# Optimization experiments

Measured on AMD Instinct MI355X. Metric: run time of the kernel, lower is better.

The kernel has to match this reference:

```python
import jax, jax.numpy as jnp
import numpy as np

B, T, E = 128, 8, 52
S, R, L = 2048, 512, 4
VOCAB = 512


def setup_inputs() -> dict:
    key = jax.random.key(0)
    ks = jax.random.split(key, 16)
    enc_len = jax.random.randint(ks[5], (B,), 0, S, dtype=jnp.int32)
    enc_len = jnp.maximum(enc_len, 1)  # ragged lengths >= 1
    return {
        "featEmbed": jax.random.normal(ks[0], (B, T, E), jnp.float32),
        "labelsEmbed": jax.random.normal(ks[1], (B, T, E), jnp.float32),
        "encoder_outputs": jax.random.normal(ks[2], (B, S, R), jnp.float32),
        "h_n": jax.random.normal(ks[3], (B, R), jnp.float32),
        "mask": jax.random.randint(ks[4], (B, T), 0, 2, dtype=jnp.int32),
        "enc_len": enc_len,
        "emb_feat_table": jax.random.normal(ks[6], (VOCAB, E), jnp.float32) * 0.1,
        "W_fc_pool": jax.random.normal(ks[7], (L, R), jnp.float32) * (1.0 / np.sqrt(R)),
        "W_reg": jax.random.normal(ks[8], (L, R), jnp.float32) * (1.0 / np.sqrt(R)),
        "b_reg": jax.random.normal(ks[9], (L,), jnp.float32) * 0.01,
        "W_ih": jax.random.normal(ks[10], (3 * R, 2 * E), jnp.float32) * (1.0 / np.sqrt(2 * E)),
        "W_hh": jax.random.normal(ks[11], (3 * R, R), jnp.float32) * (1.0 / np.sqrt(R)),
        "b_ih": jax.random.normal(ks[12], (3 * R,), jnp.float32) * 0.01,
        "b_hh": jax.random.normal(ks[13], (3 * R,), jnp.float32) * 0.01,
    }


# label -> feature-vocab remap (dict d in original forward)
REMAP = jnp.array([175, 176, 44, 173], dtype=jnp.int32)


def _gru_cell(x, h, W_ih, W_hh, b_ih, b_hh):
    # PyTorch nn.GRUCell semantics
    gi = x @ W_ih.T + b_ih  # [B, 3R]
    gh = h @ W_hh.T + b_hh
    i_r, i_z, i_n = jnp.split(gi, 3, axis=1)
    h_r, h_z, h_nn = jnp.split(gh, 3, axis=1)
    r = jax.nn.sigmoid(i_r + h_r)
    z = jax.nn.sigmoid(i_z + h_z)
    n = jnp.tanh(i_n + r * h_nn)
    return (1.0 - z) * n + z * h


def reference(featEmbed, labelsEmbed, encoder_outputs, h_n, mask, enc_len,
              emb_feat_table, W_fc_pool, W_reg, b_reg, W_ih, W_hh, b_ih, b_hh):
    S_ = encoder_outputs.shape[1]
    # Ragged max-pool over valid encoder positions (replaces per-sample AdaptiveMaxPool1d loop)
    valid = jnp.arange(S_)[None, :] < enc_len[:, None]          # [B, S]
    neg = jnp.finfo(encoder_outputs.dtype).min
    code_pool = jnp.max(jnp.where(valid[:, :, None], encoder_outputs, neg), axis=1)  # [B, R]
    a = code_pool @ W_fc_pool.T                                  # [B, L]; constant over t

    def step(h, inp):
        x, bmi_t, m = inp                                        # [B,E], [B,E], [B]
        bmi_h = h @ W_reg.T + b_reg + a                          # [B, L]
        bmi_prob = jax.nn.sigmoid(bmi_h)
        bmi_label = jnp.argmax(bmi_prob, axis=1)                 # [B]
        label_dict = REMAP[bmi_label]                            # host-dict remap, vectorized
        bmi_label_enc = emb_feat_table[label_dict]               # [B, E]
        mf = m.astype(x.dtype)[:, None]
        bmi = bmi_t * mf + (1.0 - mf) * bmi_label_enc
        h_new = _gru_cell(jnp.concatenate([x, bmi], axis=1), h, W_ih, W_hh, b_ih, b_hh)
        return h_new, (bmi_label, bmi_prob, bmi_h, label_dict)

    xs = (jnp.swapaxes(featEmbed, 0, 1),    # [T,B,E]
          jnp.swapaxes(labelsEmbed, 0, 1),  # [T,B,E]
          mask.T)                            # [T,B]
    _, (dec_output, dec_prob, disc_input, kl_input) = jax.lax.scan(step, h_n, xs)
    L_ = dec_prob.shape[-1]
    # dec_output: [T,B] labels; dec_prob: [T,B,L]; disc_input: [T*B,L]; kl_input: [T*B]
    return dec_output, dec_prob, disc_input.reshape(-1, L_), kl_input.reshape(-1)
```

## Files before the change

kernel.cpp:

```cpp
#include <hip/hip_runtime.h>
#include <float.h>
#include <math.h>


#define B_ 128
#define T_ 8
#define E_ 52
#define S_ 2048
#define R_ 512
#define L_ 4
#define GR_ 1536
#define KX_ 104
#define NCHUNK 16
#define SCHUNK (S_ / NCHUNK)
#define NQ_ 154
#define XQ_ 26

__device__ __constant__ int c_remap[4] = {175, 176, 44, 173};

__device__ __forceinline__ float sigmoidf(float x) { return 1.0f / (1.0f + expf(-x)); }
__device__ __forceinline__ float dot4(float4 w, float4 x, float a) {
    a = fmaf(w.x, x.x, a);
    a = fmaf(w.y, x.y, a);
    a = fmaf(w.z, x.z, a);
    a = fmaf(w.w, x.w, a);
    return a;
}

__global__ void k_maxpool(const float* __restrict__ enc, const int* __restrict__ enc_len,
                          float4* __restrict__ partial) {
    int c = blockIdx.x;
    int b = blockIdx.y;
    int t = threadIdx.x;
    int len = enc_len[b];
    int s0 = c * SCHUNK;
    int s1 = min(s0 + SCHUNK, len);
    float4 m = make_float4(-FLT_MAX, -FLT_MAX, -FLT_MAX, -FLT_MAX);
    const float4* base = (const float4*)(enc + (size_t)b * S_ * R_);
    for (int s = s0; s < s1; ++s) {
        float4 v = base[(size_t)s * (R_ / 4) + t];
        m.x = fmaxf(m.x, v.x);
        m.y = fmaxf(m.y, v.y);
        m.z = fmaxf(m.z, v.z);
        m.w = fmaxf(m.w, v.w);
    }
    partial[((size_t)b * NCHUNK + c) * (R_ / 4) + t] = m;
}

__global__ void k_pool_a(const float* __restrict__ partial, const float* __restrict__ W_fc,
                         float* __restrict__ a_out) {
    int b = blockIdx.x;
    int tid = threadIdx.x;
    __shared__ float cp[R_];
    for (int r = tid; r < R_; r += 256) {
        float m = -FLT_MAX;
        const float* p = partial + (size_t)b * NCHUNK * R_ + r;
        #pragma unroll
        for (int c = 0; c < NCHUNK; ++c) m = fmaxf(m, p[c * R_]);
        cp[r] = m;
    }
    __syncthreads();
    float p0 = 0.f, p1 = 0.f, p2 = 0.f, p3 = 0.f;
    for (int r = tid; r < R_; r += 256) {
        float v = cp[r];
        p0 = fmaf(v, W_fc[0 * R_ + r], p0);
        p1 = fmaf(v, W_fc[1 * R_ + r], p1);
        p2 = fmaf(v, W_fc[2 * R_ + r], p2);
        p3 = fmaf(v, W_fc[3 * R_ + r], p3);
    }
    #pragma unroll
    for (int off = 32; off > 0; off >>= 1) {
        p0 += __shfl_down(p0, off);
        p1 += __shfl_down(p1, off);
        p2 += __shfl_down(p2, off);
        p3 += __shfl_down(p3, off);
    }
    __shared__ float red[4][4];
    int wv = tid >> 6, lane = tid & 63;
    if (lane == 0) { red[wv][0] = p0; red[wv][1] = p1; red[wv][2] = p2; red[wv][3] = p3; }
    __syncthreads();
    if (tid < 4) {
        a_out[b * L_ + tid] = red[0][tid] + red[1][tid] + red[2][tid] + red[3][tid];
    }
}

__global__ void k_pack(const float* __restrict__ Wih, const float* __restrict__ Whh,
                       float4* __restrict__ Wp) {
    int qd = blockIdx.x;
    int rr = threadIdx.x;
    #pragma unroll
    for (int g = 0; g < 3; ++g) {
        int row = g * 512 + rr;
        float4 v;
        if (qd < XQ_) v = *(const float4*)(Wih + (size_t)row * KX_ + 4 * qd);
        else          v = *(const float4*)(Whh + (size_t)row * R_  + 4 * (qd - XQ_));
        Wp[((size_t)qd * 3 + g) * 512 + rr] = v;
    }
}

__global__ void __launch_bounds__(1024, 1) k_step(
        const float* __restrict__ h, const float* __restrict__ W_reg,
        const float* __restrict__ b_reg, const float* __restrict__ a_vec,
        const float* __restrict__ featEmbed, const float* __restrict__ labelsEmbed,
        const int* __restrict__ mask, const float* __restrict__ emb_table,
        const float4* __restrict__ Wp, const float* __restrict__ b_ih,
        const float* __restrict__ b_hh,
        int t, float* __restrict__ h_out, float* __restrict__ out) {
    int tid = threadIdx.x;
    int lane = tid & 63;
    int w = tid >> 6;
    int b0 = blockIdx.y * 4;
    int rr = blockIdx.x * 64 + lane;

    __shared__ __align__(16) float xs[4][KX_];
    __shared__ __align__(16) float hs[4][R_];
    __shared__ float red[8][64][17];

    if (w >= 4 && w < 8) {
        int bi = w - 4;
        const float4* src = (const float4*)(h + (size_t)(b0 + bi) * R_);
        float4* dst = (float4*)hs[bi];
        dst[lane] = src[lane];
        dst[lane + 64] = src[lane + 64];
    }

    if (w < 4) {
        int bp = b0 + w;
        const float* hb = h + (size_t)bp * R_;
        float p0 = 0.f, p1 = 0.f, p2 = 0.f, p3 = 0.f;
        #pragma unroll
        for (int r = lane; r < R_; r += 64) {
            float v = hb[r];
            p0 = fmaf(v, W_reg[r], p0);
            p1 = fmaf(v, W_reg[512 + r], p1);
            p2 = fmaf(v, W_reg[1024 + r], p2);
            p3 = fmaf(v, W_reg[1536 + r], p3);
        }
        #pragma unroll
        for (int off = 32; off > 0; off >>= 1) {
            p0 += __shfl_down(p0, off);
            p1 += __shfl_down(p1, off);
            p2 += __shfl_down(p2, off);
            p3 += __shfl_down(p3, off);
        }
        p0 = __shfl(p0, 0); p1 = __shfl(p1, 0); p2 = __shfl(p2, 0); p3 = __shfl(p3, 0);
        float bh[4];
        bh[0] = p0 + b_reg[0] + a_vec[bp * 4 + 0];
        bh[1] = p1 + b_reg[1] + a_vec[bp * 4 + 1];
        bh[2] = p2 + b_reg[2] + a_vec[bp * 4 + 2];
        bh[3] = p3 + b_reg[3] + a_vec[bp * 4 + 3];
        float pr[4];
        #pragma unroll
        for (int l = 0; l < 4; ++l) pr[l] = sigmoidf(bh[l]);
        int best = 0;
        float bv = pr[0];
        #pragma unroll
        for (int l = 1; l < 4; ++l) {
            if (pr[l] > bv) { bv = pr[l]; best = l; }
        }
        int ld = c_remap[best];
        if (blockIdx.x == 0 && lane == 0) {
            out[t * B_ + bp] = (float)best;
            #pragma unroll
            for (int l = 0; l < 4; ++l) {
                out[1024 + (t * B_ + bp) * 4 + l] = pr[l];
                out[5120 + (t * B_ + bp) * 4 + l] = bh[l];
            }
            out[9216 + t * B_ + bp] = (float)ld;
        }
        if (lane < E_) {
            xs[w][lane] = featEmbed[bp * (T_ * E_) + t * E_ + lane];
            int m = mask[bp * T_ + t];
            xs[w][E_ + lane] = m ? labelsEmbed[bp * (T_ * E_) + t * E_ + lane]
                                 : emb_table[ld * E_ + lane];
        }
    }
    __syncthreads();

    float acc[16];
    #pragma unroll
    for (int j = 0; j < 16; ++j) acc[j] = 0.f;

    int q0 = (NQ_ * w) >> 4;
    int q1 = (NQ_ * (w + 1)) >> 4;
    const float4* wp0 = Wp + (size_t)q0 * 1536 + rr;

    int xe = min(q1, XQ_);
    #pragma unroll 2
    for (int qd = q0; qd < xe; ++qd) {
        float4 wr = wp0[0];
        float4 wz = wp0[512];
        float4 wn = wp0[1024];
        wp0 += 1536;
        #pragma unroll
        for (int bi = 0; bi < 4; ++bi) {
            float4 xv = *(const float4*)&xs[bi][4 * qd];
            acc[0 + bi]  = dot4(wr, xv, acc[0 + bi]);
            acc[4 + bi]  = dot4(wz, xv, acc[4 + bi]);
            acc[8 + bi]  = dot4(wn, xv, acc[8 + bi]);
        }
    }
    int hq0 = max(q0, XQ_);
    #pragma unroll 2
    for (int qd = hq0; qd < q1; ++qd) {
        float4 wr = wp0[0];
        float4 wz = wp0[512];
        float4 wn = wp0[1024];
        wp0 += 1536;
        int hq = 4 * (qd - XQ_);
        #pragma unroll
        for (int bi = 0; bi < 4; ++bi) {
            float4 xv = *(const float4*)&hs[bi][hq];
            acc[0 + bi]  = dot4(wr, xv, acc[0 + bi]);
            acc[4 + bi]  = dot4(wz, xv, acc[4 + bi]);
            acc[12 + bi] = dot4(wn, xv, acc[12 + bi]);
        }
    }

    if (w >= 8) {
        float* d = red[w - 8][lane];
        #pragma unroll
        for (int j = 0; j < 16; ++j) d[j] = acc[j];
    }
    __syncthreads();
    if (w < 8) {
        const float* s = red[w][lane];
        #pragma unroll
        for (int j = 0; j < 16; ++j) acc[j] += s[j];
    }
    if (w >= 4 && w < 8) {
        float* d = red[w][lane];
        #pragma unroll
        for (int j = 0; j < 16; ++j) d[j] = acc[j];
    }
    __syncthreads();
    if (w < 4) {
        const float* s = red[w + 4][lane];
        #pragma unroll
        for (int j = 0; j < 16; ++j) acc[j] += s[j];
    }
    if (w >= 2 && w < 4) {
        float* d = red[w][lane];
        #pragma unroll
        for (int j = 0; j < 16; ++j) d[j] = acc[j];
    }
    __syncthreads();
    if (w < 2) {
        const float* s = red[w + 2][lane];
        #pragma unroll
        for (int j = 0; j < 16; ++j) acc[j] += s[j];
    }
    if (w == 1) {
        float* d = red[1][lane];
        #pragma unroll
        for (int j = 0; j < 16; ++j) d[j] = acc[j];
    }
    __syncthreads();
    if (w == 0) {
        const float* s = red[1][lane];
        #pragma unroll
        for (int j = 0; j < 16; ++j) acc[j] += s[j];
        float bir = b_ih[rr],        bhr = b_hh[rr];
        float biz = b_ih[512 + rr],  bhz = b_hh[512 + rr];
        float bin = b_ih[1024 + rr], bhn = b_hh[1024 + rr];
        #pragma unroll
        for (int bi = 0; bi < 4; ++bi) {
            float r = sigmoidf(acc[0 + bi] + bir + bhr);
            float z = sigmoidf(acc[4 + bi] + biz + bhz);
            float n = tanhf(acc[8 + bi] + bin + r * (acc[12 + bi] + bhn));
            h_out[(size_t)(b0 + bi) * R_ + rr] = (1.0f - z) * n + z * hs[bi][rr];
        }
    }
}

extern "C" void kernel_launch(void* const* d_in, const int* in_sizes, int n_in,
                              void* d_out, int out_size, void* d_ws, size_t ws_size,
                              hipStream_t stream) {
    const float* featEmbed   = (const float*)d_in[0];
    const float* labelsEmbed = (const float*)d_in[1];
    const float* enc         = (const float*)d_in[2];
    const float* h_n         = (const float*)d_in[3];
    const int*   mask        = (const int*)d_in[4];
    const int*   enc_len     = (const int*)d_in[5];
    const float* emb_table   = (const float*)d_in[6];
    const float* W_fc        = (const float*)d_in[7];
    const float* W_reg       = (const float*)d_in[8];
    const float* b_reg       = (const float*)d_in[9];
    const float* W_ih        = (const float*)d_in[10];
    const float* W_hh        = (const float*)d_in[11];
    const float* b_ih        = (const float*)d_in[12];
    const float* b_hh        = (const float*)d_in[13];
    float* out = (float*)d_out;

    float* ws      = (float*)d_ws;
    float* partial = ws;
    float* Wp      = partial + B_ * NCHUNK * R_;
    float* h0      = Wp + NQ_ * 3 * R_ * 4;
    float* h1      = h0 + B_ * R_;
    float* a_vec   = h1 + B_ * R_;

    k_pack<<<dim3(NQ_), 512, 0, stream>>>(W_ih, W_hh, (float4*)Wp);
    k_maxpool<<<dim3(NCHUNK, B_), 128, 0, stream>>>(enc, enc_len, (float4*)partial);
    k_pool_a<<<B_, 256, 0, stream>>>(partial, W_fc, a_vec);

    const float* hcur = h_n;
    for (int t = 0; t < T_; ++t) {
        float* hnext = (t & 1) ? h1 : h0;
        k_step<<<dim3(R_ / 64, B_ / 4), 1024, 0, stream>>>(
            hcur, W_reg, b_reg, a_vec, featEmbed, labelsEmbed, mask, emb_table,
            (const float4*)Wp, b_ih, b_hh, t, hnext, out);
        hcur = hnext;
    }
}
```

Before: 773.9 us.

## Fuse weight pack into maxpool kernel and retile GRU step to 8 batches × 32 rows

```diff
diff --git a/kernel.cpp b/kernel.cpp
--- a/kernel.cpp
+++ b/kernel.cpp
@@ -27,24 +27,43 @@
     return a;
 }
 
-__global__ void k_maxpool(const float* __restrict__ enc, const int* __restrict__ enc_len,
-                          float4* __restrict__ partial) {
-    int c = blockIdx.x;
-    int b = blockIdx.y;
-    int t = threadIdx.x;
+__global__ void k_pool_pack(const float* __restrict__ enc, const int* __restrict__ enc_len,
+                            float4* __restrict__ partial,
+                            const float* __restrict__ Wih, const float* __restrict__ Whh,
+                            float4* __restrict__ Wp) {
+    int idx = blockIdx.x;
+    int tid = threadIdx.x;
+    if (idx >= NCHUNK * B_) {
+        int qd = idx - NCHUNK * B_;
+        #pragma unroll
+        for (int i = 0; i < 4; ++i) {
+            int rr = tid + 128 * i;
+            #pragma unroll
+            for (int g = 0; g < 3; ++g) {
+                int row = g * 512 + rr;
+                float4 v;
+                if (qd < XQ_) v = *(const float4*)(Wih + (size_t)row * KX_ + 4 * qd);
+                else          v = *(const float4*)(Whh + (size_t)row * R_  + 4 * (qd - XQ_));
+                Wp[((size_t)qd * 3 + g) * 512 + rr] = v;
+            }
+        }
+        return;
+    }
+    int c = idx & (NCHUNK - 1);
+    int b = idx >> 4;
     int len = enc_len[b];
     int s0 = c * SCHUNK;
     int s1 = min(s0 + SCHUNK, len);
     float4 m = make_float4(-FLT_MAX, -FLT_MAX, -FLT_MAX, -FLT_MAX);
     const float4* base = (const float4*)(enc + (size_t)b * S_ * R_);
     for (int s = s0; s < s1; ++s) {
-        float4 v = base[(size_t)s * (R_ / 4) + t];
+        float4 v = base[(size_t)s * (R_ / 4) + tid];
         m.x = fmaxf(m.x, v.x);
         m.y = fmaxf(m.y, v.y);
         m.z = fmaxf(m.z, v.z);
         m.w = fmaxf(m.w, v.w);
     }
-    partial[((size_t)b * NCHUNK + c) * (R_ / 4) + t] = m;
+    partial[((size_t)b * NCHUNK + c) * (R_ / 4) + tid] = m;
 }
 
 __global__ void k_pool_a(const float* __restrict__ partial, const float* __restrict__ W_fc,
@@ -81,20 +100,6 @@
     __syncthreads();
     if (tid < 4) {
         a_out[b * L_ + tid] = red[0][tid] + red[1][tid] + red[2][tid] + red[3][tid];
-    }
-}
-
-__global__ void k_pack(const float* __restrict__ Wih, const float* __restrict__ Whh,
-                       float4* __restrict__ Wp) {
-    int qd = blockIdx.x;
-    int rr = threadIdx.x;
-    #pragma unroll
-    for (int g = 0; g < 3; ++g) {
-        int row = g * 512 + rr;
-        float4 v;
-        if (qd < XQ_) v = *(const float4*)(Wih + (size_t)row * KX_ + 4 * qd);
-        else          v = *(const float4*)(Whh + (size_t)row * R_  + 4 * (qd - XQ_));
-        Wp[((size_t)qd * 3 + g) * 512 + rr] = v;
     }
 }
 
@@ -109,22 +114,24 @@
     int tid = threadIdx.x;
     int lane = tid & 63;
     int w = tid >> 6;
-    int b0 = blockIdx.y * 4;
-    int rr = blockIdx.x * 64 + lane;
-
-    __shared__ __align__(16) float xs[4][KX_];
-    __shared__ __align__(16) float hs[4][R_];
+    int b0 = blockIdx.y * 8;
+    int rrl = lane & 31;
+    int bh = lane >> 5;
+    int rr = blockIdx.x * 32 + rrl;
+
+    __shared__ __align__(16) float xs[8][KX_];
+    __shared__ __align__(16) float hs[8][R_];
     __shared__ float red[8][64][17];
 
-    if (w >= 4 && w < 8) {
-        int bi = w - 4;
+    if (w >= 8) {
+        int bi = w - 8;
         const float4* src = (const float4*)(h + (size_t)(b0 + bi) * R_);
         float4* dst = (float4*)hs[bi];
         dst[lane] = src[lane];
         dst[lane + 64] = src[lane + 64];
     }
 
-    if (w < 4) {
+    if (w < 8) {
         int bp = b0 + w;
         const float* hb = h + (size_t)bp * R_;
         float p0 = 0.f, p1 = 0.f, p2 = 0.f, p3 = 0.f;
@@ -144,14 +151,14 @@
             p3 += __shfl_down(p3, off);
         }
         p0 = __shfl(p0, 0); p1 = __shfl(p1, 0); p2 = __shfl(p2, 0); p3 = __shfl(p3, 0);
-        float bh[4];
-        bh[0] = p0 + b_reg[0] + a_vec[bp * 4 + 0];
-        bh[1] = p1 + b_reg[1] + a_vec[bp * 4 + 1];
-        bh[2] = p2 + b_reg[2] + a_vec[bp * 4 + 2];
-        bh[3] = p3 + b_reg[3] + a_vec[bp * 4 + 3];
+        float bh_[4];
+        bh_[0] = p0 + b_reg[0] + a_vec[bp * 4 + 0];
+        bh_[1] = p1 + b_reg[1] + a_vec[bp * 4 + 1];
+        bh_[2] = p2 + b_reg[2] + a_vec[bp * 4 + 2];
+        bh_[3] = p3 + b_reg[3] + a_vec[bp * 4 + 3];
         float pr[4];
         #pragma unroll
-        for (int l = 0; l < 4; ++l) pr[l] = sigmoidf(bh[l]);
+        for (int l = 0; l < 4; ++l) pr[l] = sigmoidf(bh_[l]);
         int best = 0;
         float bv = pr[0];
         #pragma unroll
@@ -164,7 +171,7 @@
             #pragma unroll
             for (int l = 0; l < 4; ++l) {
                 out[1024 + (t * B_ + bp) * 4 + l] = pr[l];
-                out[5120 + (t * B_ + bp) * 4 + l] = bh[l];
+                out[5120 + (t * B_ + bp) * 4 + l] = bh_[l];
             }
             out[9216 + t * B_ + bp] = (float)ld;
         }
@@ -193,11 +200,11 @@
         float4 wn = wp0[1024];
         wp0 += 1536;
         #pragma unroll
-        for (int bi = 0; bi < 4; ++bi) {
-            float4 xv = *(const float4*)&xs[bi][4 * qd];
-            acc[0 + bi]  = dot4(wr, xv, acc[0 + bi]);
-            acc[4 + bi]  = dot4(wz, xv, acc[4 + bi]);
-            acc[8 + bi]  = dot4(wn, xv, acc[8 + bi]);
+        for (int i = 0; i < 4; ++i) {
+            float4 xv = *(const float4*)&xs[bh * 4 + i][4 * qd];
+            acc[0 + i] = dot4(wr, xv, acc[0 + i]);
+            acc[4 + i] = dot4(wz, xv, acc[4 + i]);
+            acc[8 + i] = dot4(wn, xv, acc[8 + i]);
         }
     }
     int hq0 = max(q0, XQ_);
@@ -209,11 +216,11 @@
         wp0 += 1536;
         int hq = 4 * (qd - XQ_);
         #pragma unroll
-        for (int bi = 0; bi < 4; ++bi) {
-            float4 xv = *(const float4*)&hs[bi][hq];
-            acc[0 + bi]  = dot4(wr, xv, acc[0 + bi]);
-            acc[4 + bi]  = dot4(wz, xv, acc[4 + bi]);
-            acc[12 + bi] = dot4(wn, xv, acc[12 + bi]);
+        for (int i = 0; i < 4; ++i) {
+            float4 xv = *(const float4*)&hs[bh * 4 + i][hq];
+            acc[0 + i]  = dot4(wr, xv, acc[0 + i]);
+            acc[4 + i]  = dot4(wz, xv, acc[4 + i]);
+            acc[12 + i] = dot4(wn, xv, acc[12 + i]);
         }
     }
 
@@ -264,10 +271,11 @@
         float biz = b_ih[512 + rr],  bhz = b_hh[512 + rr];
         float bin = b_ih[1024 + rr], bhn = b_hh[1024 + rr];
         #pragma unroll
-        for (int bi = 0; bi < 4; ++bi) {
-            float r = sigmoidf(acc[0 + bi] + bir + bhr);
-            float z = sigmoidf(acc[4 + bi] + biz + bhz);
-            float n = tanhf(acc[8 + bi] + bin + r * (acc[12 + bi] + bhn));
+        for (int i = 0; i < 4; ++i) {
+            int bi = bh * 4 + i;
+            float r = sigmoidf(acc[0 + i] + bir + bhr);
+            float z = sigmoidf(acc[4 + i] + biz + bhz);
+            float n = tanhf(acc[8 + i] + bin + r * (acc[12 + i] + bhn));
             h_out[(size_t)(b0 + bi) * R_ + rr] = (1.0f - z) * n + z * hs[bi][rr];
         }
     }
@@ -299,14 +307,14 @@
     float* h1      = h0 + B_ * R_;
     float* a_vec   = h1 + B_ * R_;
 
-    k_pack<<<dim3(NQ_), 512, 0, stream>>>(W_ih, W_hh, (float4*)Wp);
-    k_maxpool<<<dim3(NCHUNK, B_), 128, 0, stream>>>(enc, enc_len, (float4*)partial);
+    k_pool_pack<<<dim3(NCHUNK * B_ + NQ_), 128, 0, stream>>>(
+        enc, enc_len, (float4*)partial, W_ih, W_hh, (float4*)Wp);
     k_pool_a<<<B_, 256, 0, stream>>>(partial, W_fc, a_vec);
 
     const float* hcur = h_n;
     for (int t = 0; t < T_; ++t) {
         float* hnext = (t & 1) ? h1 : h0;
-        k_step<<<dim3(R_ / 64, B_ / 4), 1024, 0, stream>>>(
+        k_step<<<dim3(R_ / 32, B_ / 8), 1024, 0, stream>>>(
             hcur, W_reg, b_reg, a_vec, featEmbed, labelsEmbed, mask, emb_table,
             (const float4*)Wp, b_ih, b_hh, t, hnext, out);
         hcur = hnext;
```

After: 765.4 us. No clear change (-1.1%).
